# Kernel tuning notes

Measured on AMD Instinct MI355X. Metric: run time of the kernel, lower is better.

## Reference

```python
import jax, jax.numpy as jnp
import numpy as np

B, T, V, E, H, O = 4096, 5, 8192, 32, 512, 1024
LN_EPS = 1e-5


def _ln(x, g, b):
    m = x.mean(-1, keepdims=True)
    v = x.var(-1, keepdims=True)
    return (x - m) / jnp.sqrt(v + LN_EPS) * g + b


def setup_inputs() -> dict:
    key = jax.random.key(0)
    ks = jax.random.split(key, 8)
    s_emb = 1.0 / np.sqrt(V)
    s_gru = 1.0 / np.sqrt(H)
    s_fc = 1.0 / np.sqrt(H)
    return {
        "message": jax.random.normal(ks[0], (B, T, V), jnp.float32),
        "emb_W": jax.random.normal(ks[1], (E, V), jnp.float32) * s_emb,
        "emb_b": jnp.zeros((E,), jnp.float32),
        "init_emb": jax.random.normal(ks[2], (1, E), jnp.float32),
        "eln_g": jnp.ones((E,), jnp.float32),
        "eln_b": jnp.zeros((E,), jnp.float32),
        "Wih": jax.random.normal(ks[3], (3 * H, E), jnp.float32) * s_gru,
        "Whh": jax.random.normal(ks[4], (3 * H, H), jnp.float32) * s_gru,
        "bih": jnp.zeros((3 * H,), jnp.float32),
        "bhh": jnp.zeros((3 * H,), jnp.float32),
        "gln_g": jnp.ones((H,), jnp.float32),
        "gln_b": jnp.zeros((H,), jnp.float32),
        "fc_W": jax.random.normal(ks[5], (O, H), jnp.float32) * s_fc,
        "fc_b": jnp.zeros((O,), jnp.float32),
    }


def reference(message, emb_W, emb_b, init_emb, eln_g, eln_b,
              Wih, Whh, bih, bhh, gln_g, gln_b, fc_W, fc_b):
    # embed all message steps at once: [B, T, E]
    emb = _ln(jnp.einsum('btv,ev->bte', message, emb_W) + emb_b, eln_g, eln_b)
    # GRU input sequence: LN(initial_embedding), then embeddings of steps 0..T-2
    x0 = jnp.broadcast_to(_ln(init_emb, eln_g, eln_b), (B, E))
    xs = jnp.concatenate([x0[None], jnp.swapaxes(emb[:, :T - 1], 0, 1)], axis=0)  # [T, B, E]

    def step(h, x):
        gi = x @ Wih.T + bih            # [B, 3H]
        gh = h @ Whh.T + bhh            # [B, 3H]
        ir, iz, inn = jnp.split(gi, 3, axis=-1)
        hr, hz, hn = jnp.split(gh, 3, axis=-1)
        r = jax.nn.sigmoid(ir + hr)
        z = jax.nn.sigmoid(iz + hz)
        n = jnp.tanh(inn + r * hn)
        h_new = (1.0 - z) * n + z * h
        return h_new, None

    h_last, _ = jax.lax.scan(step, jnp.zeros((B, H), message.dtype), xs)
    # eval mode: GaussianDropout is identity
    return jax.nn.sigmoid(_ln(h_last, gln_g, gln_b) @ fc_W.T + fc_b)
```

## Files before the change

### kernel.cpp

```cpp
#include <hip/hip_runtime.h>
#include <hip/hip_bf16.h>
#include <math.h>


#define LN_EPS 1e-5f

typedef __attribute__((ext_vector_type(8))) short bf8;
typedef __attribute__((ext_vector_type(4))) float fx4;

__device__ __forceinline__ float bf2f(short s) {
    union { unsigned u; float f; } v;
    v.u = ((unsigned)(unsigned short)s) << 16;
    return v.f;
}
__device__ __forceinline__ short f2bf(float f) {
    union { __hip_bfloat16 h; unsigned short u; } v;
    v.h = __float2bfloat16(f);
    return (short)v.u;
}
__device__ __forceinline__ float sigmoidf(float x) { return 1.0f / (1.0f + expf(-x)); }

__global__ __launch_bounds__(256) void k_prep(
    const float* __restrict__ Whh, const float* __restrict__ Wih,
    const float* __restrict__ fcW, const float* __restrict__ embW,
    const float* __restrict__ init_emb, const float* __restrict__ eln_g,
    const float* __restrict__ eln_b,
    short* __restrict__ Whh_bf, short* __restrict__ Wih_bf,
    short* __restrict__ fcW_bf, short* __restrict__ embW_bf,
    short* __restrict__ x0v, short* __restrict__ h0)
{
    int gid = blockIdx.x * blockDim.x + threadIdx.x;
    int stride = gridDim.x * blockDim.x;
    for (int i = gid; i < 1536 * 512; i += stride) Whh_bf[i] = f2bf(Whh[i]);
    for (int i = gid; i < 1536 * 32;  i += stride) Wih_bf[i] = f2bf(Wih[i]);
    for (int i = gid; i < 1024 * 512; i += stride) fcW_bf[i] = f2bf(fcW[i]);
    for (int i = gid; i < 32 * 8192;  i += stride) embW_bf[i] = f2bf(embW[i]);
    int* h0i = (int*)h0;
    for (int i = gid; i < 4096 * 512 / 2; i += stride) h0i[i] = 0;
    if (blockIdx.x == 0 && threadIdx.x < 32) {
        float v = init_emb[threadIdx.x];
        float s = v, q = v * v;
        #pragma unroll
        for (int m = 1; m < 32; m <<= 1) { s += __shfl_xor(s, m); q += __shfl_xor(q, m); }
        float mean = s * (1.0f / 32.0f);
        float var  = q * (1.0f / 32.0f) - mean * mean;
        float rstd = rsqrtf(var + LN_EPS);
        x0v[threadIdx.x] = f2bf((v - mean) * rstd * eln_g[threadIdx.x] + eln_b[threadIdx.x]);
    }
}

__global__ __launch_bounds__(256) void k_embed(
    const float* __restrict__ msg, const short* __restrict__ embW_bf,
    const float* __restrict__ emb_b, const float* __restrict__ eln_g,
    const float* __restrict__ eln_b, short* __restrict__ xs)
{
    __shared__ short As[64][72];
    __shared__ short Bs[32][72];
    __shared__ float Cs[64][33];

    const int tid  = threadIdx.x;
    const int wid  = tid >> 6;
    const int lane = tid & 63;
    const int m    = lane & 15;
    const int quad = lane >> 4;
    const int row0 = blockIdx.x * 64;

    fx4 acc[2];
    #pragma unroll
    for (int i = 0; i < 2; ++i)
        #pragma unroll
        for (int j = 0; j < 4; ++j) acc[i][j] = 0.0f;

    for (int k0 = 0; k0 < 8192; k0 += 64) {
        #pragma unroll
        for (int i = 0; i < 2; ++i) {
            int c = tid + i * 256;
            int r = c >> 3, kp = (c & 7) * 8;
            int rg = row0 + r;
            int b = rg >> 2, t = rg & 3;
            const float* src = msg + (size_t)(b * 5 + t) * 8192 + k0 + kp;
            float4 a0 = *(const float4*)src;
            float4 a1 = *(const float4*)(src + 4);
            short* d = &As[r][kp];
            d[0] = f2bf(a0.x); d[1] = f2bf(a0.y); d[2] = f2bf(a0.z); d[3] = f2bf(a0.w);
            d[4] = f2bf(a1.x); d[5] = f2bf(a1.y); d[6] = f2bf(a1.z); d[7] = f2bf(a1.w);
        }
        {
            int c = tid;
            int n = c >> 3, kp = (c & 7) * 8;
            *(bf8*)&Bs[n][kp] = *(const bf8*)(embW_bf + (size_t)n * 8192 + k0 + kp);
        }
        __syncthreads();
        #pragma unroll
        for (int kk = 0; kk < 64; kk += 32) {
            bf8 a  = *(const bf8*)&As[wid * 16 + m][kk + quad * 8];
            bf8 b0 = *(const bf8*)&Bs[m][kk + quad * 8];
            bf8 b1 = *(const bf8*)&Bs[16 + m][kk + quad * 8];
            acc[0] = __builtin_amdgcn_mfma_f32_16x16x32_bf16(a, b0, acc[0], 0, 0, 0);
            acc[1] = __builtin_amdgcn_mfma_f32_16x16x32_bf16(a, b1, acc[1], 0, 0, 0);
        }
        __syncthreads();
    }
    #pragma unroll
    for (int nt = 0; nt < 2; ++nt)
        #pragma unroll
        for (int r = 0; r < 4; ++r)
            Cs[wid * 16 + quad * 4 + r][nt * 16 + m] = acc[nt][r];
    __syncthreads();
    if (tid < 64) {
        int rg = row0 + tid;
        int b = rg >> 2, t = rg & 3;
        float sum = 0.f, sq = 0.f;
        for (int e = 0; e < 32; ++e) {
            float v = Cs[tid][e] + emb_b[e];
            sum += v; sq += v * v;
        }
        float mean = sum * (1.0f / 32.0f);
        float var  = sq * (1.0f / 32.0f) - mean * mean;
        float rstd = rsqrtf(var + LN_EPS);
        short* dst = xs + (size_t)(t + 1) * 131072 + (size_t)b * 32;
        for (int e = 0; e < 32; ++e) {
            float v = Cs[tid][e] + emb_b[e];
            dst[e] = f2bf((v - mean) * rstd * eln_g[e] + eln_b[e]);
        }
    }
}

__global__ __launch_bounds__(256) void k_gru_step(
    const short* __restrict__ x, int x_stride,
    const short* __restrict__ h_in, short* __restrict__ h_out,
    const short* __restrict__ Whh_bf, const short* __restrict__ Wih_bf,
    const float* __restrict__ bih, const float* __restrict__ bhh)
{
    __shared__ short Hs[64][72];
    __shared__ short Ws[96][72];
    __shared__ short Xs[64][40];
    __shared__ short WIs[96][40];

    const int tid  = threadIdx.x;
    const int wid  = tid >> 6;
    const int lane = tid & 63;
    const int m    = lane & 15;
    const int quad = lane >> 4;
    const int row0 = blockIdx.x * 64;
    const int j0   = blockIdx.y * 32;

    fx4 acc_h[6], acc_i[6];
    #pragma unroll
    for (int i = 0; i < 6; ++i)
        #pragma unroll
        for (int j = 0; j < 4; ++j) { acc_h[i][j] = 0.0f; acc_i[i][j] = 0.0f; }

    {
        int c = tid;
        int r = c >> 2, kp = (c & 3) * 8;
        const short* src = x + (size_t)(row0 + r) * x_stride + kp;
        *(bf8*)&Xs[r][kp] = *(const bf8*)src;
    }
    #pragma unroll
    for (int i = 0; i < 2; ++i) {
        int c = tid + i * 256;
        if (c < 384) {
            int n = c >> 2, kp = (c & 3) * 8;
            int s = n >> 5, jj = n & 31;
            int g = s * 512 + j0 + jj;
            *(bf8*)&WIs[n][kp] = *(const bf8*)(Wih_bf + (size_t)g * 32 + kp);
        }
    }

    for (int k0 = 0; k0 < 512; k0 += 64) {
        #pragma unroll
        for (int i = 0; i < 2; ++i) {
            int c = tid + i * 256;
            int r = c >> 3, kp = (c & 7) * 8;
            *(bf8*)&Hs[r][kp] = *(const bf8*)(h_in + (size_t)(row0 + r) * 512 + k0 + kp);
        }
        #pragma unroll
        for (int i = 0; i < 3; ++i) {
            int c = tid + i * 256;
            int n = c >> 3, kp = (c & 7) * 8;
            int s = n >> 5, jj = n & 31;
            int g = s * 512 + j0 + jj;
            *(bf8*)&Ws[n][kp] = *(const bf8*)(Whh_bf + (size_t)g * 512 + k0 + kp);
        }
        __syncthreads();
        #pragma unroll
        for (int kk = 0; kk < 64; kk += 32) {
            bf8 a = *(const bf8*)&Hs[wid * 16 + m][kk + quad * 8];
            #pragma unroll
            for (int nt = 0; nt < 6; ++nt) {
                bf8 b = *(const bf8*)&Ws[(nt >> 1) * 32 + (nt & 1) * 16 + m][kk + quad * 8];
                acc_h[nt] = __builtin_amdgcn_mfma_f32_16x16x32_bf16(a, b, acc_h[nt], 0, 0, 0);
            }
        }
        __syncthreads();
    }
    {
        bf8 a = *(const bf8*)&Xs[wid * 16 + m][quad * 8];
        #pragma unroll
        for (int nt = 0; nt < 6; ++nt) {
            bf8 b = *(const bf8*)&WIs[(nt >> 1) * 32 + (nt & 1) * 16 + m][quad * 8];
            acc_i[nt] = __builtin_amdgcn_mfma_f32_16x16x32_bf16(a, b, acc_i[nt], 0, 0, 0);
        }
    }
    #pragma unroll
    for (int nt = 0; nt < 2; ++nt) {
        #pragma unroll
        for (int r = 0; r < 4; ++r) {
            int j  = j0 + nt * 16 + m;
            int rg = row0 + wid * 16 + quad * 4 + r;
            float rpre = acc_i[0 + nt][r] + bih[j]        + acc_h[0 + nt][r] + bhh[j];
            float zpre = acc_i[2 + nt][r] + bih[512 + j]  + acc_h[2 + nt][r] + bhh[512 + j];
            float inn  = acc_i[4 + nt][r] + bih[1024 + j];
            float hn   = acc_h[4 + nt][r] + bhh[1024 + j];
            float rr = sigmoidf(rpre);
            float zz = sigmoidf(zpre);
            float nn = tanhf(inn + rr * hn);
            float ho = bf2f(h_in[(size_t)rg * 512 + j]);
            h_out[(size_t)rg * 512 + j] = f2bf((1.0f - zz) * nn + zz * ho);
        }
    }
}

__global__ __launch_bounds__(256) void k_hln(
    const short* __restrict__ h, const float* __restrict__ g,
    const float* __restrict__ b, short* __restrict__ hln)
{
    int wid = threadIdx.x >> 6, lane = threadIdx.x & 63;
    int row = blockIdx.x * 4 + wid;
    bf8 v = *(const bf8*)(h + (size_t)row * 512 + lane * 8);
    float f[8];
    float sum = 0.f, sq = 0.f;
    #pragma unroll
    for (int i = 0; i < 8; ++i) { f[i] = bf2f(v[i]); sum += f[i]; sq += f[i] * f[i]; }
    #pragma unroll
    for (int msk = 1; msk < 64; msk <<= 1) { sum += __shfl_xor(sum, msk); sq += __shfl_xor(sq, msk); }
    float mean = sum * (1.0f / 512.0f);
    float var  = sq * (1.0f / 512.0f) - mean * mean;
    float rstd = rsqrtf(var + LN_EPS);
    short o[8];
    #pragma unroll
    for (int i = 0; i < 8; ++i) {
        int col = lane * 8 + i;
        o[i] = f2bf((f[i] - mean) * rstd * g[col] + b[col]);
    }
    *(bf8*)(hln + (size_t)row * 512 + lane * 8) = *(bf8*)o;
}

__global__ __launch_bounds__(256) void k_fc(
    const short* __restrict__ hln, const short* __restrict__ fcW_bf,
    const float* __restrict__ fc_b, float* __restrict__ out)
{
    __shared__ short As[64][72];
    __shared__ short Bs[64][72];

    const int tid  = threadIdx.x;
    const int wid  = tid >> 6;
    const int lane = tid & 63;
    const int m    = lane & 15;
    const int quad = lane >> 4;
    const int row0 = blockIdx.x * 64;
    const int col0 = blockIdx.y * 64;

    fx4 acc[4];
    #pragma unroll
    for (int i = 0; i < 4; ++i)
        #pragma unroll
        for (int j = 0; j < 4; ++j) acc[i][j] = 0.0f;

    for (int k0 = 0; k0 < 512; k0 += 64) {
        #pragma unroll
        for (int i = 0; i < 2; ++i) {
            int c = tid + i * 256;
            int r = c >> 3, kp = (c & 7) * 8;
            *(bf8*)&As[r][kp] = *(const bf8*)(hln + (size_t)(row0 + r) * 512 + k0 + kp);
        }
        #pragma unroll
        for (int i = 0; i < 2; ++i) {
            int c = tid + i * 256;
            int n = c >> 3, kp = (c & 7) * 8;
            *(bf8*)&Bs[n][kp] = *(const bf8*)(fcW_bf + (size_t)(col0 + n) * 512 + k0 + kp);
        }
        __syncthreads();
        #pragma unroll
        for (int kk = 0; kk < 64; kk += 32) {
            bf8 a = *(const bf8*)&As[wid * 16 + m][kk + quad * 8];
            #pragma unroll
            for (int nt = 0; nt < 4; ++nt) {
                bf8 b = *(const bf8*)&Bs[nt * 16 + m][kk + quad * 8];
                acc[nt] = __builtin_amdgcn_mfma_f32_16x16x32_bf16(a, b, acc[nt], 0, 0, 0);
            }
        }
        __syncthreads();
    }
    #pragma unroll
    for (int nt = 0; nt < 4; ++nt) {
        #pragma unroll
        for (int r = 0; r < 4; ++r) {
            int col = col0 + nt * 16 + m;
            int rg  = row0 + wid * 16 + quad * 4 + r;
            float v = acc[nt][r] + fc_b[col];
            out[(size_t)rg * 1024 + col] = sigmoidf(v);
        }
    }
}

extern "C" void kernel_launch(void* const* d_in, const int* in_sizes, int n_in,
                              void* d_out, int out_size, void* d_ws, size_t ws_size,
                              hipStream_t stream)
{
    const float* msg      = (const float*)d_in[0];
    const float* embW     = (const float*)d_in[1];
    const float* emb_b    = (const float*)d_in[2];
    const float* init_emb = (const float*)d_in[3];
    const float* eln_g    = (const float*)d_in[4];
    const float* eln_b    = (const float*)d_in[5];
    const float* Wih      = (const float*)d_in[6];
    const float* Whh      = (const float*)d_in[7];
    const float* bih      = (const float*)d_in[8];
    const float* bhh      = (const float*)d_in[9];
    const float* gln_g    = (const float*)d_in[10];
    const float* gln_b    = (const float*)d_in[11];
    const float* fcW      = (const float*)d_in[12];
    const float* fc_b     = (const float*)d_in[13];
    float* out = (float*)d_out;

    short* base    = (short*)d_ws;
    short* Whh_bf  = base;
    short* Wih_bf  = Whh_bf + 1536 * 512;
    short* fcW_bf  = Wih_bf + 1536 * 32;
    short* embW_bf = fcW_bf + 1024 * 512;
    short* xs      = embW_bf + 32 * 8192;
    short* h0      = xs + 5 * 4096 * 32;
    short* h1      = h0 + 4096 * 512;
    short* hln     = h1 + 4096 * 512;
    short* x0v     = hln + 4096 * 512;

    k_prep<<<512, 256, 0, stream>>>(Whh, Wih, fcW, embW, init_emb, eln_g, eln_b,
                                    Whh_bf, Wih_bf, fcW_bf, embW_bf, x0v, h0);
    k_embed<<<256, 256, 0, stream>>>(msg, embW_bf, emb_b, eln_g, eln_b, xs);

    short* hi = h0;
    short* ho = h1;
    for (int t = 0; t < 5; ++t) {
        const short* xp = (t == 0) ? x0v : xs + (size_t)t * 4096 * 32;
        int xstride = (t == 0) ? 0 : 32;
        k_gru_step<<<dim3(64, 16), 256, 0, stream>>>(xp, xstride, hi, ho,
                                                     Whh_bf, Wih_bf, bih, bhh);
        short* tmp = hi; hi = ho; ho = tmp;
    }
    k_hln<<<1024, 256, 0, stream>>>(hi, gln_g, gln_b, hln);
    k_fc<<<dim3(64, 16), 256, 0, stream>>>(hln, fcW_bf, fc_b, out);
}
```

Measured before the change: 996.1 us.

## Split embedding GEMM over K across waves with direct register loads

The embedding projection kernel now gives each block 16 rows instead of 64 and splits the 8192-long reduction across the four waves. Each wave loads message rows and embedding weights straight from global memory into MFMA operands, with no shared-memory staging and no per-iteration barriers. Partial sums are reduced through shared memory, and the layer norm is done with a wavefront shuffle reduction. This raises the grid from 256 to 1024 blocks to expose more memory parallelism on the bandwidth-bound message read. In exchange, global loads are less coalesced (16 rows by 32 bytes per wave load), and the embedding weights are re-read by four times as many blocks.

```diff
diff --git a/kernel.cpp b/kernel.cpp
--- a/kernel.cpp
+++ b/kernel.cpp
@@ -54,74 +54,68 @@
     const float* __restrict__ emb_b, const float* __restrict__ eln_g,
     const float* __restrict__ eln_b, short* __restrict__ xs)
 {
-    __shared__ short As[64][72];
-    __shared__ short Bs[32][72];
-    __shared__ float Cs[64][33];
+    __shared__ float part[4][16][33];
 
     const int tid  = threadIdx.x;
-    const int wid  = tid >> 6;
+    const int w    = tid >> 6;
     const int lane = tid & 63;
     const int m    = lane & 15;
     const int quad = lane >> 4;
-    const int row0 = blockIdx.x * 64;
-
-    fx4 acc[2];
-    #pragma unroll
-    for (int i = 0; i < 2; ++i)
-        #pragma unroll
-        for (int j = 0; j < 4; ++j) acc[i][j] = 0.0f;
-
-    for (int k0 = 0; k0 < 8192; k0 += 64) {
-        #pragma unroll
-        for (int i = 0; i < 2; ++i) {
-            int c = tid + i * 256;
-            int r = c >> 3, kp = (c & 7) * 8;
-            int rg = row0 + r;
-            int b = rg >> 2, t = rg & 3;
-            const float* src = msg + (size_t)(b * 5 + t) * 8192 + k0 + kp;
-            float4 a0 = *(const float4*)src;
-            float4 a1 = *(const float4*)(src + 4);
-            short* d = &As[r][kp];
-            d[0] = f2bf(a0.x); d[1] = f2bf(a0.y); d[2] = f2bf(a0.z); d[3] = f2bf(a0.w);
-            d[4] = f2bf(a1.x); d[5] = f2bf(a1.y); d[6] = f2bf(a1.z); d[7] = f2bf(a1.w);
-        }
-        {
-            int c = tid;
-            int n = c >> 3, kp = (c & 7) * 8;
-            *(bf8*)&Bs[n][kp] = *(const bf8*)(embW_bf + (size_t)n * 8192 + k0 + kp);
-        }
-        __syncthreads();
-        #pragma unroll
-        for (int kk = 0; kk < 64; kk += 32) {
-            bf8 a  = *(const bf8*)&As[wid * 16 + m][kk + quad * 8];
-            bf8 b0 = *(const bf8*)&Bs[m][kk + quad * 8];
-            bf8 b1 = *(const bf8*)&Bs[16 + m][kk + quad * 8];
-            acc[0] = __builtin_amdgcn_mfma_f32_16x16x32_bf16(a, b0, acc[0], 0, 0, 0);
-            acc[1] = __builtin_amdgcn_mfma_f32_16x16x32_bf16(a, b1, acc[1], 0, 0, 0);
-        }
-        __syncthreads();
-    }
-    #pragma unroll
-    for (int nt = 0; nt < 2; ++nt)
-        #pragma unroll
-        for (int r = 0; r < 4; ++r)
-            Cs[wid * 16 + quad * 4 + r][nt * 16 + m] = acc[nt][r];
+
+    const int rg = blockIdx.x * 16 + m;
+    const int b  = rg >> 2, t = rg & 3;
+    const float* __restrict__ row = msg + (size_t)(b * 5 + t) * 8192;
+
+    const short* __restrict__ bw0 = embW_bf + (size_t)m * 8192;
+    const short* __restrict__ bw1 = embW_bf + (size_t)(16 + m) * 8192;
+
+    fx4 acc0, acc1;
+    #pragma unroll
+    for (int j = 0; j < 4; ++j) { acc0[j] = 0.0f; acc1[j] = 0.0f; }
+
+    const int kbeg = w * 2048;
+    const int kend = kbeg + 2048;
+    #pragma unroll 4
+    for (int k0 = kbeg; k0 < kend; k0 += 32) {
+        const int kq = k0 + quad * 8;
+        float4 a0 = *(const float4*)(row + kq);
+        float4 a1 = *(const float4*)(row + kq + 4);
+        bf8 a;
+        a[0] = f2bf(a0.x); a[1] = f2bf(a0.y); a[2] = f2bf(a0.z); a[3] = f2bf(a0.w);
+        a[4] = f2bf(a1.x); a[5] = f2bf(a1.y); a[6] = f2bf(a1.z); a[7] = f2bf(a1.w);
+        bf8 b0 = *(const bf8*)(bw0 + kq);
+        bf8 b1 = *(const bf8*)(bw1 + kq);
+        acc0 = __builtin_amdgcn_mfma_f32_16x16x32_bf16(a, b0, acc0, 0, 0, 0);
+        acc1 = __builtin_amdgcn_mfma_f32_16x16x32_bf16(a, b1, acc1, 0, 0, 0);
+    }
+
+    #pragma unroll
+    for (int r = 0; r < 4; ++r) {
+        part[w][quad * 4 + r][m]      = acc0[r];
+        part[w][quad * 4 + r][16 + m] = acc1[r];
+    }
     __syncthreads();
-    if (tid < 64) {
-        int rg = row0 + tid;
-        int b = rg >> 2, t = rg & 3;
-        float sum = 0.f, sq = 0.f;
-        for (int e = 0; e < 32; ++e) {
-            float v = Cs[tid][e] + emb_b[e];
-            sum += v; sq += v * v;
-        }
-        float mean = sum * (1.0f / 32.0f);
-        float var  = sq * (1.0f / 32.0f) - mean * mean;
-        float rstd = rsqrtf(var + LN_EPS);
-        short* dst = xs + (size_t)(t + 1) * 131072 + (size_t)b * 32;
-        for (int e = 0; e < 32; ++e) {
-            float v = Cs[tid][e] + emb_b[e];
-            dst[e] = f2bf((v - mean) * rstd * eln_g[e] + eln_b[e]);
+
+    {
+        const int rr = tid >> 5;
+        const int c  = tid & 31;
+        #pragma unroll
+        for (int half = 0; half < 2; ++half) {
+            const int r = rr + half * 8;
+            float v = part[0][r][c] + part[1][r][c] + part[2][r][c] + part[3][r][c]
+                    + emb_b[c];
+            float s = v, q = v * v;
+            #pragma unroll
+            for (int msk = 1; msk < 32; msk <<= 1) {
+                s += __shfl_xor(s, msk); q += __shfl_xor(q, msk);
+            }
+            float mean = s * (1.0f / 32.0f);
+            float var  = q * (1.0f / 32.0f) - mean * mean;
+            float rstd = rsqrtf(var + LN_EPS);
+            const int rg2 = blockIdx.x * 16 + r;
+            const int b2 = rg2 >> 2, t2 = rg2 & 3;
+            xs[(size_t)(t2 + 1) * 131072 + (size_t)b2 * 32 + c] =
+                f2bf((v - mean) * rstd * eln_g[c] + eln_b[c]);
         }
     }
 }
@@ -338,7 +332,7 @@
 
     k_prep<<<512, 256, 0, stream>>>(Whh, Wih, fcW, embW, init_emb, eln_g, eln_b,
                                     Whh_bf, Wih_bf, fcW_bf, embW_bf, x0v, h0);
-    k_embed<<<256, 256, 0, stream>>>(msg, embW_bf, emb_b, eln_g, eln_b, xs);
+    k_embed<<<1024, 256, 0, stream>>>(msg, embW_bf, emb_b, eln_g, eln_b, xs);
 
     short* hi = h0;
     short* ho = h1;
```

After: 948.6 us. 4.8% less time.
